# Kernel optimization log

Hardware: AMD Instinct MI355X
Metric: run time of the kernel (lower is better)

Reference implementation:

```python
import jax, jax.numpy as jnp
import numpy as np

EPS = 1e-6

def _rotate(z, q):
    # rotation trick (Householder-style reflection chain), z,q: [M, D]
    sg = jax.lax.stop_gradient
    z_norm = z / (jnp.linalg.norm(z, axis=1, keepdims=True) + EPS)
    q_norm = q / (jnp.linalg.norm(q, axis=1, keepdims=True) + EPS)
    w = sg((z_norm + q_norm) / jnp.linalg.norm(z_norm + q_norm, axis=1, keepdims=True))
    zn_d = sg(z_norm)
    qn_d = sg(q_norm)
    e = z - 2.0 * jnp.sum(z * w, axis=1, keepdims=True) * w \
          + 2.0 * jnp.sum(z * zn_d, axis=1, keepdims=True) * qn_d
    scale = sg(jnp.linalg.norm(q, axis=1, keepdims=True) / (jnp.linalg.norm(z, axis=1, keepdims=True) + EPS))
    return e * scale

def setup_inputs() -> dict:
    key = jax.random.key(0)
    k1, k2 = jax.random.split(key)
    x = jax.random.normal(k1, (16, 2048, 512), dtype=jnp.float32)
    codebooks = jax.random.normal(k2, (8, 1024, 512), dtype=jnp.float32)
    return {"x": x, "codebooks": codebooks}

def reference(x, codebooks):
    # x: [B, N, D]; codebooks: [Q, C, D]
    B, N, D = x.shape
    Q, C, _ = codebooks.shape
    sg = jax.lax.stop_gradient
    cb_sq = jnp.sum(codebooks * codebooks, axis=-1)  # [Q, C]
    residual = x
    quantized_out = jnp.zeros_like(x)
    all_indices = []
    all_losses = []
    for qi in range(Q):
        cb = codebooks[qi]                               # [C, D]
        flat = residual.reshape(-1, D)                   # [B*N, D]
        # squared euclidean distance: ||r||^2 - 2 r.c + ||c||^2
        d2 = jnp.sum(flat * flat, axis=1, keepdims=True) - 2.0 * (flat @ cb.T) + cb_sq[qi]
        ind = jnp.argmin(d2, axis=1)                     # [B*N]
        quant_raw = jnp.take(cb, ind, axis=0)            # [B*N, D]
        # commitment loss (codebook frozen per freeze_codebook=True)
        loss = jnp.mean((sg(quant_raw) - flat) ** 2)
        # rotation-trick transform of the quantized vectors
        quant = _rotate(flat, quant_raw).reshape(B, N, D)
        residual = residual - sg(quant)
        quantized_out = quantized_out + quant
        all_indices.append(ind.reshape(B, N))
        all_losses.append(loss)
    all_indices = jnp.stack(all_indices, axis=-1)        # [B, N, Q]
    all_losses = jnp.stack(all_losses, axis=-1)          # [Q]
    return quantized_out, all_indices, all_losses
```

## Files before the change

### kernel.cpp

```cpp
#include <hip/hip_runtime.h>

#define EPS 1e-6f

typedef __attribute__((ext_vector_type(8))) short bf16x8;
typedef __attribute__((ext_vector_type(4))) float f32x4;
typedef __attribute__((ext_vector_type(8))) unsigned short ushort8;

#define AS1(p) ((const __attribute__((address_space(1))) void*)(p))
#define AS3(p) ((__attribute__((address_space(3))) void*)(p))

__device__ inline unsigned int fkey(float f) {
  unsigned int u = __float_as_uint(f);
  return (u & 0x80000000u) ? ~u : (u | 0x80000000u);
}

__device__ inline unsigned long long shfl_xor_u64(unsigned long long v, int mask) {
  unsigned int lo = (unsigned int)(v & 0xffffffffull);
  unsigned int hi = (unsigned int)(v >> 32);
  lo = (unsigned int)__shfl_xor((int)lo, mask);
  hi = (unsigned int)__shfl_xor((int)hi, mask);
  return (((unsigned long long)hi) << 32) | lo;
}

__device__ inline unsigned short f2bf(float f) {
  unsigned int u = __float_as_uint(f);
  u += 0x7fffu + ((u >> 16) & 1u);
  return (unsigned short)(u >> 16);
}
__device__ inline float bf2f(unsigned short h) {
  return __uint_as_float(((unsigned int)h) << 16);
}

__device__ inline unsigned lds_off(const void* p) {
  return (unsigned)(unsigned long long)(__attribute__((address_space(3))) const void*)p;
}

template<int OFF>
__device__ inline bf16x8 ds_read128(unsigned addr) {
  bf16x8 r;
  asm volatile("ds_read_b128 %0, %1 offset:%2" : "=v"(r) : "v"(addr), "i"(OFF));
  return r;
}

template<int OFF>
__device__ inline float gload_f32(unsigned long long a) {
  float r;
  asm volatile("global_load_dword %0, %1, off offset:%2" : "=v"(r) : "v"(a), "i"(OFF));
  return r;
}

__global__ __launch_bounds__(256) void prep_kernel(
    const float* __restrict__ x, const float* __restrict__ cbs,
    unsigned short* __restrict__ Rhi, unsigned short* __restrict__ Rlo,
    unsigned short* __restrict__ CBhi, unsigned short* __restrict__ CBlo,
    float* __restrict__ cbsq, float* __restrict__ loss_out) {
  constexpr size_t M = 32768, D = 512, C = 1024, Q = 8;
  const size_t nthreads = (size_t)gridDim.x * 256;
  const size_t gtid = (size_t)blockIdx.x * 256 + threadIdx.x;
  const int lane = threadIdx.x & 63;
  const int w = threadIdx.x >> 6;

  for (size_t i = gtid; i < M * D / 8; i += nthreads) {
    size_t off = i * 8;
    float4 v0 = *(const float4*)(x + off);
    float4 v1 = *(const float4*)(x + off + 4);
    float v[8] = {v0.x, v0.y, v0.z, v0.w, v1.x, v1.y, v1.z, v1.w};
    ushort8 h, l;
    #pragma unroll
    for (int j = 0; j < 8; j++) {
      unsigned short hh = f2bf(v[j]);
      h[j] = hh;
      l[j] = f2bf(v[j] - bf2f(hh));
    }
    *(ushort8*)(Rhi + off) = h;
    *(ushort8*)(Rlo + off) = l;
  }
  for (size_t i = gtid; i < Q * C * D / 8; i += nthreads) {
    size_t off = i * 8;
    float4 v0 = *(const float4*)(cbs + off);
    float4 v1 = *(const float4*)(cbs + off + 4);
    float v[8] = {v0.x, v0.y, v0.z, v0.w, v1.x, v1.y, v1.z, v1.w};
    ushort8 h, l;
    #pragma unroll
    for (int j = 0; j < 8; j++) {
      unsigned short hh = f2bf(v[j]);
      h[j] = hh;
      l[j] = f2bf(v[j] - bf2f(hh));
    }
    *(ushort8*)(CBhi + off) = h;
    *(ushort8*)(CBlo + off) = l;
  }
  for (int row = blockIdx.x * 4 + w; row < (int)(Q * C); row += gridDim.x * 4) {
    const float4* p = (const float4*)(cbs + (size_t)row * 512);
    float4 v0 = p[lane];
    float4 v1 = p[lane + 64];
    float s = v0.x*v0.x + v0.y*v0.y + v0.z*v0.z + v0.w*v0.w
            + v1.x*v1.x + v1.y*v1.y + v1.z*v1.z + v1.w*v1.w;
    #pragma unroll
    for (int off = 32; off; off >>= 1) s += __shfl_xor(s, off);
    if (lane == 0) cbsq[row] = s;
  }
  if (blockIdx.x == 0 && threadIdx.x < (int)Q) loss_out[threadIdx.x] = 0.f;
}

__global__ __launch_bounds__(512, 2) void stage_kernel(
    const float* __restrict__ x, const float* __restrict__ cbq_f32,
    unsigned short* __restrict__ Rhi, unsigned short* __restrict__ Rlo,
    const unsigned short* __restrict__ Chi, const unsigned short* __restrict__ Clo,
    const float* __restrict__ cq_base, float* __restrict__ qout,
    float* __restrict__ idx_out, float* __restrict__ loss_out,
    int qi, int last) {
  __shared__ unsigned short As[3][2][128 * 32];
  __shared__ unsigned short Bs[3][2][256 * 32];
  __shared__ unsigned long long bestLDS[4][128];
  __shared__ float ls[8];

  const int tid = threadIdx.x;
  const int lane = tid & 63;
  const int w = tid >> 6;
  const int wr = w >> 2, wc = w & 3;
  const int row0 = blockIdx.x * 128;

  const int rw = lane >> 2, oq = lane & 3;
  const int o_sw = (oq - rw - (rw >> 2)) & 3;
  const int m = lane & 15, g = lane >> 4;
  const int f_sw8 = ((g + m + (m >> 2)) & 3) * 8;

  const unsigned short* pAhi = Rhi + (size_t)(row0 + w * 16 + rw) * 512 + o_sw * 8;
  const unsigned short* pAlo = Rlo + (size_t)(row0 + w * 16 + rw) * 512 + o_sw * 8;
  const unsigned short* pBhi = Chi + (size_t)(w * 32 + rw) * 512 + o_sw * 8;
  const unsigned short* pBlo = Clo + (size_t)(w * 32 + rw) * 512 + o_sw * 8;

  unsigned aA = lds_off(&As[0][0][(wr * 64 + m) * 32 + f_sw8]);
  unsigned aB = lds_off(&Bs[0][0][(wc * 64 + m) * 32 + f_sw8]);

  unsigned long long best[4][4];
  #pragma unroll
  for (int mi = 0; mi < 4; mi++)
    #pragma unroll
    for (int r = 0; r < 4; r++) best[mi][r] = ~0ull;

  auto stage = [&](int buf, int t) {
    const size_t ko = (size_t)((t & 15) * 32);
    const size_t cof = (size_t)((t >> 4) * 256) * 512;
    unsigned short* dAh = &As[buf][0][w * 512];
    unsigned short* dAl = &As[buf][1][w * 512];
    unsigned short* dBh = &Bs[buf][0][w * 1024];
    unsigned short* dBl = &Bs[buf][1][w * 1024];
    __builtin_amdgcn_global_load_lds(AS1(pAhi + ko), AS3(dAh), 16, 0, 0);
    __builtin_amdgcn_global_load_lds(AS1(pAlo + ko), AS3(dAl), 16, 0, 0);
    __builtin_amdgcn_global_load_lds(AS1(pBhi + cof + ko), AS3(dBh), 16, 0, 0);
    __builtin_amdgcn_global_load_lds(AS1(pBhi + cof + ko + 8192), AS3(dBh + 512), 16, 0, 0);
    __builtin_amdgcn_global_load_lds(AS1(pBlo + cof + ko), AS3(dBl), 16, 0, 0);
    __builtin_amdgcn_global_load_lds(AS1(pBlo + cof + ko + 8192), AS3(dBl + 512), 16, 0, 0);
  };

  float cq[4][4];
  {
    unsigned long long cqp = (unsigned long long)(cq_base + wc * 64 + m);
    cq[0][0] = gload_f32<0>(cqp);    cq[0][1] = gload_f32<64>(cqp);
    cq[0][2] = gload_f32<128>(cqp);  cq[0][3] = gload_f32<192>(cqp);
    cq[1][0] = gload_f32<1024>(cqp); cq[1][1] = gload_f32<1088>(cqp);
    cq[1][2] = gload_f32<1152>(cqp); cq[1][3] = gload_f32<1216>(cqp);
    cq[2][0] = gload_f32<2048>(cqp); cq[2][1] = gload_f32<2112>(cqp);
    cq[2][2] = gload_f32<2176>(cqp); cq[2][3] = gload_f32<2240>(cqp);
    cq[3][0] = gload_f32<3072>(cqp); cq[3][1] = gload_f32<3136>(cqp);
    cq[3][2] = gload_f32<3200>(cqp); cq[3][3] = gload_f32<3264>(cqp);
    asm volatile("s_waitcnt vmcnt(0)" ::: "memory");
  }

  bf16x8 f0_ah[4], f0_al[4], f0_bh[4], f0_bl[4];
  bf16x8 f1_ah[4], f1_al[4], f1_bh[4], f1_bl[4];
  f32x4 acc[4][4];
  int bn = 0;
  int bst = 0;

  stage(0, 0);
  asm volatile("s_waitcnt vmcnt(0)" ::: "memory");
  asm volatile("s_barrier" ::: "memory");
  __builtin_amdgcn_sched_barrier(0);

  f0_ah[0] = ds_read128<0>(aA);     f0_ah[1] = ds_read128<1024>(aA);
  f0_ah[2] = ds_read128<2048>(aA);  f0_ah[3] = ds_read128<3072>(aA);
  f0_al[0] = ds_read128<8192>(aA);  f0_al[1] = ds_read128<9216>(aA);
  f0_al[2] = ds_read128<10240>(aA); f0_al[3] = ds_read128<11264>(aA);
  f0_bh[0] = ds_read128<0>(aB);     f0_bh[1] = ds_read128<1024>(aB);
  f0_bh[2] = ds_read128<2048>(aB);  f0_bh[3] = ds_read128<3072>(aB);
  f0_bl[0] = ds_read128<16384>(aB); f0_bl[1] = ds_read128<17408>(aB);
  f0_bl[2] = ds_read128<18432>(aB); f0_bl[3] = ds_read128<19456>(aB);
  aA += 16384; aB += 32768; bn = 1;

  stage(1, 1);
  stage(2, 2);
  asm volatile("s_waitcnt lgkmcnt(0)" ::: "memory");
  asm volatile("s_waitcnt vmcnt(6)" ::: "memory");
  asm volatile("s_barrier" ::: "memory");
  __builtin_amdgcn_sched_barrier(0);

#define K_ITER(T, RD, CS)                                                        \
  {                                                                              \
    const int t_ = (T);                                                          \
    if (t_ < 63) {                  \
      RD##_ah[0] = ds_read128<0>(aA);     RD##_ah[1] = ds_read128<1024>(aA);     \
      RD##_ah[2] = ds_read128<2048>(aA);  RD##_ah[3] = ds_read128<3072>(aA);     \
      RD##_al[0] = ds_read128<8192>(aA);  RD##_al[1] = ds_read128<9216>(aA);     \
      RD##_al[2] = ds_read128<10240>(aA); RD##_al[3] = ds_read128<11264>(aA);    \
      RD##_bh[0] = ds_read128<0>(aB);     RD##_bh[1] = ds_read128<1024>(aB);     \
      RD##_bh[2] = ds_read128<2048>(aB);  RD##_bh[3] = ds_read128<3072>(aB);     \
      RD##_bl[0] = ds_read128<16384>(aB); RD##_bl[1] = ds_read128<17408>(aB);    \
      RD##_bl[2] = ds_read128<18432>(aB); RD##_bl[3] = ds_read128<19456>(aB);    \
      const int s_ = (bn == 2) ? -2 : 1;                                         \
      aA += s_ * 16384; aB += s_ * 32768; bn = (bn == 2) ? 0 : bn + 1;           \
    }                                                                            \
    if (t_ < 61) stage(bst, t_ + 3);                                             \
    bst = (bst == 2) ? 0 : bst + 1;                                              \
    __builtin_amdgcn_sched_barrier(0);                                           \
    if ((t_ & 15) == 0) {                                                        \
      _Pragma("unroll") for (int mi = 0; mi < 4; mi++)                           \
        _Pragma("unroll") for (int ni = 0; ni < 4; ni++)                         \
          acc[mi][ni] = (f32x4){0.f, 0.f, 0.f, 0.f};                             \
    }                                                                            \
    __builtin_amdgcn_s_setprio(1);                                               \
    _Pragma("unroll") for (int mi = 0; mi < 4; mi++)                             \
      _Pragma("unroll") for (int ni = 0; ni < 4; ni++)                           \
        acc[mi][ni] = __builtin_amdgcn_mfma_f32_16x16x32_bf16(                   \
            CS##_ah[mi], CS##_bh[ni], acc[mi][ni], 0, 0, 0);                     \
    _Pragma("unroll") for (int mi = 0; mi < 4; mi++)                             \
      _Pragma("unroll") for (int ni = 0; ni < 4; ni++)                           \
        acc[mi][ni] = __builtin_amdgcn_mfma_f32_16x16x32_bf16(                   \
            CS##_ah[mi], CS##_bl[ni], acc[mi][ni], 0, 0, 0);                     \
    _Pragma("unroll") for (int mi = 0; mi < 4; mi++)                             \
      _Pragma("unroll") for (int ni = 0; ni < 4; ni++)                           \
        acc[mi][ni] = __builtin_amdgcn_mfma_f32_16x16x32_bf16(                   \
            CS##_al[mi], CS##_bh[ni], acc[mi][ni], 0, 0, 0);                     \
    __builtin_amdgcn_s_setprio(0);                                               \
    if ((t_ & 15) == 15) {       \
      const int ct_ = t_ >> 4;                                                   \
      const unsigned colb = ct_ * 256 + wc * 64 + m;                             \
      _Pragma("unroll") for (int mi = 0; mi < 4; mi++)                           \
        _Pragma("unroll") for (int r = 0; r < 4; r++) {                          \
          _Pragma("unroll") for (int ni = 0; ni < 4; ni++) {                     \
            float d2 = fmaf(-2.f, acc[mi][ni][r], cq[ct_][ni]);                  \
            unsigned long long p =                                               \
                (((unsigned long long)fkey(d2)) << 32) | (colb + ni * 16);       \
            if (p < best[mi][r]) best[mi][r] = p;                                \
          }                                                                      \
        }                                                                        \
    }                                                                            \
    asm volatile("s_waitcnt lgkmcnt(0)" ::: "memory");                           \
    if (t_ < 61) asm volatile("s_waitcnt vmcnt(6)" ::: "memory");                \
    else         asm volatile("s_waitcnt vmcnt(0)" ::: "memory");                \
    asm volatile("s_barrier" ::: "memory");                                      \
    __builtin_amdgcn_sched_barrier(0);                                           \
  }

  for (int tp = 0; tp < 32; tp++) {
    K_ITER(tp * 2,     f1, f0);
    K_ITER(tp * 2 + 1, f0, f1);
  }
#undef K_ITER

  #pragma unroll
  for (int mi = 0; mi < 4; mi++)
    #pragma unroll
    for (int r = 0; r < 4; r++) {
      unsigned long long mn = best[mi][r];
      #pragma unroll
      for (int off = 1; off < 16; off <<= 1) {
        unsigned long long o = shfl_xor_u64(mn, off);
        if (o < mn) mn = o;
      }
      best[mi][r] = mn;
    }

  if (m == 0) {
    #pragma unroll
    for (int mi = 0; mi < 4; mi++)
      #pragma unroll
      for (int r = 0; r < 4; r++)
        bestLDS[wc][wr * 64 + mi * 16 + g * 4 + r] = best[mi][r];
  }
  __syncthreads();

  float lossacc = 0.f;
  for (int rr = 0; rr < 16; rr++) {
    const int row128 = w * 16 + rr;
    unsigned long long mn = bestLDS[0][row128];
    #pragma unroll
    for (int q2 = 1; q2 < 4; q2++) {
      unsigned long long o = bestLDS[q2][row128];
      if (o < mn) mn = o;
    }
    const int c = (int)(mn & 0xffffffffu);
    const int row = row0 + row128;
    if (lane == 0) idx_out[(size_t)row * 8 + qi] = (float)c;

    const size_t base = (size_t)row * 512 + lane * 8;
    ushort8 h = *(const ushort8*)(Rhi + base);
    ushort8 l = *(const ushort8*)(Rlo + base);
    const float* qrow = cbq_f32 + (size_t)c * 512 + lane * 8;
    float4 q0 = *(const float4*)qrow;
    float4 q1 = *(const float4*)(qrow + 4);
    float z[8], q[8] = {q0.x, q0.y, q0.z, q0.w, q1.x, q1.y, q1.z, q1.w};
    #pragma unroll
    for (int j = 0; j < 8; j++) z[j] = bf2f(h[j]) + bf2f(l[j]);

    float zz = 0.f, qq = 0.f, zq = 0.f;
    #pragma unroll
    for (int j = 0; j < 8; j++) {
      zz = fmaf(z[j], z[j], zz);
      qq = fmaf(q[j], q[j], qq);
      zq = fmaf(z[j], q[j], zq);
    }
    #pragma unroll
    for (int off = 32; off; off >>= 1) {
      zz += __shfl_xor(zz, off);
      qq += __shfl_xor(qq, off);
      zq += __shfl_xor(zq, off);
    }

    float nz = sqrtf(zz), nq = sqrtf(qq);
    float inz = 1.f / (nz + EPS), inq = 1.f / (nq + EPS);
    float ns  = sqrtf(zz*inz*inz + 2.f*zq*inz*inq + qq*inq*inq);
    float ins = 1.f / ns;
    float zw  = (zz*inz + zq*inq) * ins;
    float zzn = zz * inz;
    float scale = nq * inz;
    float az = scale * (1.f - 2.f * zw * ins * inz);
    float aq = scale * (2.f * zzn - 2.f * zw * ins) * inq;

    if (!last) {
      #pragma unroll
      for (int j = 0; j < 8; j++) {
        float r = z[j] - (az * z[j] + aq * q[j]);
        unsigned short hh = f2bf(r);
        h[j] = hh;
        l[j] = f2bf(r - bf2f(hh));
      }
      *(ushort8*)(Rhi + base) = h;
      *(ushort8*)(Rlo + base) = l;
    } else {
      float4 x0 = *(const float4*)(x + base);
      float4 x1 = *(const float4*)(x + base + 4);
      float xv[8] = {x0.x, x0.y, x0.z, x0.w, x1.x, x1.y, x1.z, x1.w};
      float o[8];
      #pragma unroll
      for (int j = 0; j < 8; j++) {
        float r = z[j] - (az * z[j] + aq * q[j]);
        o[j] = xv[j] - r;
      }
      *(float4*)(qout + base)     = (float4){o[0], o[1], o[2], o[3]};
      *(float4*)(qout + base + 4) = (float4){o[4], o[5], o[6], o[7]};
    }
    lossacc += (zz - 2.f * zq + qq);
  }
  if (lane == 0) ls[w] = lossacc;
  __syncthreads();
  if (tid == 0)
    atomicAdd(loss_out + qi, (ls[0] + ls[1] + ls[2] + ls[3] +
                              ls[4] + ls[5] + ls[6] + ls[7]) *
                             (1.f / (32768.f * 512.f)));
}

extern "C" void kernel_launch(void* const* d_in, const int* in_sizes, int n_in,
                              void* d_out, int out_size, void* d_ws, size_t ws_size,
                              hipStream_t stream) {
  const float* x   = (const float*)d_in[0];
  const float* cbs = (const float*)d_in[1];
  float* out = (float*)d_out;
  const size_t M = 32768, D = 512, Q = 8, C = 1024;
  float* qout     = out;
  float* idx_out  = out + M * D;
  float* loss_out = idx_out + M * Q;

  unsigned short* Rhi  = (unsigned short*)d_ws;
  unsigned short* Rlo  = Rhi + M * D;
  unsigned short* CBhi = Rlo + M * D;
  unsigned short* CBlo = CBhi + Q * C * D;
  float* cbsq = (float*)(CBlo + Q * C * D);

  prep_kernel<<<512, 256, 0, stream>>>(x, cbs, Rhi, Rlo, CBhi, CBlo, cbsq, loss_out);

  for (int qi = 0; qi < (int)Q; qi++) {
    stage_kernel<<<256, 512, 0, stream>>>(
        x, cbs + (size_t)qi * C * D, Rhi, Rlo,
        CBhi + (size_t)qi * C * D, CBlo + (size_t)qi * C * D,
        cbsq + qi * C, qout, idx_out, loss_out, qi, qi == (int)Q - 1 ? 1 : 0);
  }
}
```

Before: 1.200 ms.

## Load codebook MFMA fragments directly from global memory, bypassing LDS

The codebook (B operand) tiles are no longer staged through the triple-buffered shared-memory ring. Each wave now issues global_load_dwordx4 straight into its MFMA fragment registers, one K-step ahead, and the vmcnt waits are adjusted to match. This frees most of the shared memory and removes the B-side LDS writes and reads. In exchange, global/L2 latency is exposed with only one step of prefetch, and waves that share the same codebook columns now load them redundantly from global memory.

```diff
diff --git a/kernel.cpp b/kernel.cpp
--- a/kernel.cpp
+++ b/kernel.cpp
@@ -39,6 +39,12 @@
 __device__ inline bf16x8 ds_read128(unsigned addr) {
   bf16x8 r;
   asm volatile("ds_read_b128 %0, %1 offset:%2" : "=v"(r) : "v"(addr), "i"(OFF));
+  return r;
+}
+
+__device__ inline bf16x8 gload_frag(const unsigned short* sbase, unsigned voff) {
+  bf16x8 r;
+  asm volatile("global_load_dwordx4 %0, %1, %2" : "=v"(r) : "v"(voff), "s"(sbase));
   return r;
 }
 
@@ -111,7 +117,6 @@
     float* __restrict__ idx_out, float* __restrict__ loss_out,
     int qi, int last) {
   __shared__ unsigned short As[3][2][128 * 32];
-  __shared__ unsigned short Bs[3][2][256 * 32];
   __shared__ unsigned long long bestLDS[4][128];
   __shared__ float ls[8];
 
@@ -128,11 +133,13 @@
 
   const unsigned short* pAhi = Rhi + (size_t)(row0 + w * 16 + rw) * 512 + o_sw * 8;
   const unsigned short* pAlo = Rlo + (size_t)(row0 + w * 16 + rw) * 512 + o_sw * 8;
-  const unsigned short* pBhi = Chi + (size_t)(w * 32 + rw) * 512 + o_sw * 8;
-  const unsigned short* pBlo = Clo + (size_t)(w * 32 + rw) * 512 + o_sw * 8;
+
+  unsigned voff0 = (unsigned)(((wc * 64 + m) * 512 + g * 8) * 2);
+  unsigned voff1 = voff0 + 16384u;
+  unsigned voff2 = voff0 + 32768u;
+  unsigned voff3 = voff0 + 49152u;
 
   unsigned aA = lds_off(&As[0][0][(wr * 64 + m) * 32 + f_sw8]);
-  unsigned aB = lds_off(&Bs[0][0][(wc * 64 + m) * 32 + f_sw8]);
 
   unsigned long long best[4][4];
   #pragma unroll
@@ -142,17 +149,10 @@
 
   auto stage = [&](int buf, int t) {
     const size_t ko = (size_t)((t & 15) * 32);
-    const size_t cof = (size_t)((t >> 4) * 256) * 512;
     unsigned short* dAh = &As[buf][0][w * 512];
     unsigned short* dAl = &As[buf][1][w * 512];
-    unsigned short* dBh = &Bs[buf][0][w * 1024];
-    unsigned short* dBl = &Bs[buf][1][w * 1024];
     __builtin_amdgcn_global_load_lds(AS1(pAhi + ko), AS3(dAh), 16, 0, 0);
     __builtin_amdgcn_global_load_lds(AS1(pAlo + ko), AS3(dAl), 16, 0, 0);
-    __builtin_amdgcn_global_load_lds(AS1(pBhi + cof + ko), AS3(dBh), 16, 0, 0);
-    __builtin_amdgcn_global_load_lds(AS1(pBhi + cof + ko + 8192), AS3(dBh + 512), 16, 0, 0);
-    __builtin_amdgcn_global_load_lds(AS1(pBlo + cof + ko), AS3(dBl), 16, 0, 0);
-    __builtin_amdgcn_global_load_lds(AS1(pBlo + cof + ko + 8192), AS3(dBl + 512), 16, 0, 0);
   };
 
   float cq[4][4];
@@ -180,37 +180,40 @@
   asm volatile("s_barrier" ::: "memory");
   __builtin_amdgcn_sched_barrier(0);
 
+  f0_bh[0] = gload_frag(Chi, voff0); f0_bh[1] = gload_frag(Chi, voff1);
+  f0_bh[2] = gload_frag(Chi, voff2); f0_bh[3] = gload_frag(Chi, voff3);
+  f0_bl[0] = gload_frag(Clo, voff0); f0_bl[1] = gload_frag(Clo, voff1);
+  f0_bl[2] = gload_frag(Clo, voff2); f0_bl[3] = gload_frag(Clo, voff3);
+  voff0 += 64u; voff1 += 64u; voff2 += 64u; voff3 += 64u;
   f0_ah[0] = ds_read128<0>(aA);     f0_ah[1] = ds_read128<1024>(aA);
   f0_ah[2] = ds_read128<2048>(aA);  f0_ah[3] = ds_read128<3072>(aA);
   f0_al[0] = ds_read128<8192>(aA);  f0_al[1] = ds_read128<9216>(aA);
   f0_al[2] = ds_read128<10240>(aA); f0_al[3] = ds_read128<11264>(aA);
-  f0_bh[0] = ds_read128<0>(aB);     f0_bh[1] = ds_read128<1024>(aB);
-  f0_bh[2] = ds_read128<2048>(aB);  f0_bh[3] = ds_read128<3072>(aB);
-  f0_bl[0] = ds_read128<16384>(aB); f0_bl[1] = ds_read128<17408>(aB);
-  f0_bl[2] = ds_read128<18432>(aB); f0_bl[3] = ds_read128<19456>(aB);
-  aA += 16384; aB += 32768; bn = 1;
+  aA += 16384; bn = 1;
 
   stage(1, 1);
   stage(2, 2);
   asm volatile("s_waitcnt lgkmcnt(0)" ::: "memory");
-  asm volatile("s_waitcnt vmcnt(6)" ::: "memory");
+  asm volatile("s_waitcnt vmcnt(2)" ::: "memory");
   asm volatile("s_barrier" ::: "memory");
   __builtin_amdgcn_sched_barrier(0);
 
 #define K_ITER(T, RD, CS)                                                        \
   {                                                                              \
     const int t_ = (T);                                                          \
-    if (t_ < 63) {                  \
+    if (t_ < 63) {    \
+      RD##_bh[0] = gload_frag(Chi, voff0); RD##_bh[1] = gload_frag(Chi, voff1);  \
+      RD##_bh[2] = gload_frag(Chi, voff2); RD##_bh[3] = gload_frag(Chi, voff3);  \
+      RD##_bl[0] = gload_frag(Clo, voff0); RD##_bl[1] = gload_frag(Clo, voff1);  \
+      RD##_bl[2] = gload_frag(Clo, voff2); RD##_bl[3] = gload_frag(Clo, voff3);  \
+      const unsigned d_ = ((t_ & 15) == 14) ? 261184u : 64u;                     \
+      voff0 += d_; voff1 += d_; voff2 += d_; voff3 += d_;                        \
       RD##_ah[0] = ds_read128<0>(aA);     RD##_ah[1] = ds_read128<1024>(aA);     \
       RD##_ah[2] = ds_read128<2048>(aA);  RD##_ah[3] = ds_read128<3072>(aA);     \
       RD##_al[0] = ds_read128<8192>(aA);  RD##_al[1] = ds_read128<9216>(aA);     \
       RD##_al[2] = ds_read128<10240>(aA); RD##_al[3] = ds_read128<11264>(aA);    \
-      RD##_bh[0] = ds_read128<0>(aB);     RD##_bh[1] = ds_read128<1024>(aB);     \
-      RD##_bh[2] = ds_read128<2048>(aB);  RD##_bh[3] = ds_read128<3072>(aB);     \
-      RD##_bl[0] = ds_read128<16384>(aB); RD##_bl[1] = ds_read128<17408>(aB);    \
-      RD##_bl[2] = ds_read128<18432>(aB); RD##_bl[3] = ds_read128<19456>(aB);    \
       const int s_ = (bn == 2) ? -2 : 1;                                         \
-      aA += s_ * 16384; aB += s_ * 32768; bn = (bn == 2) ? 0 : bn + 1;           \
+      aA += s_ * 16384; bn = (bn == 2) ? 0 : bn + 1;                             \
     }                                                                            \
     if (t_ < 61) stage(bst, t_ + 3);                                             \
     bst = (bst == 2) ? 0 : bst + 1;                                              \
@@ -248,8 +251,8 @@
         }                                                                        \
     }                                                                            \
     asm volatile("s_waitcnt lgkmcnt(0)" ::: "memory");                           \
-    if (t_ < 61) asm volatile("s_waitcnt vmcnt(6)" ::: "memory");                \
-    else         asm volatile("s_waitcnt vmcnt(0)" ::: "memory");                \
+    if (t_ <= 60) asm volatile("s_waitcnt vmcnt(2)" ::: "memory");               \
+    else          asm volatile("s_waitcnt vmcnt(0)" ::: "memory");               \
     asm volatile("s_barrier" ::: "memory");                                      \
     __builtin_amdgcn_sched_barrier(0);                                           \
   }
```

Result: slower. 1.527 ms (+27.3%).
